# Optimization experiments

Measured on AMD Instinct MI355X. Metric: run time of the kernel, lower is better.

Reference implementation:

```python
import jax, jax.numpy as jnp
import numpy as np

B, N, D = 8, 2048, 1024


def setup_inputs() -> dict:
    key = jax.random.key(0)
    k1, k2, k3, k4 = jax.random.split(key, 4)
    x = jax.random.normal(k1, (B, N, D), dtype=jnp.float32)
    f = jax.random.normal(k2, (B, N, D), dtype=jnp.float32)
    # nn.Linear(D, 1, bias=False) weights, shape [1, D]
    lim = 1.0 / np.sqrt(D)
    wk = jax.random.uniform(k3, (1, D), dtype=jnp.float32, minval=-lim, maxval=lim)
    wq = jax.random.uniform(k4, (1, D), dtype=jnp.float32, minval=-lim, maxval=lim)
    return {"x": x, "f": f, "wk": wk, "wq": wq}


def reference(x, f, wk, wq):
    # scalar k/q projections: [B, N]
    k = jnp.einsum("bnd,d->bn", x, wk[0])
    q = jnp.einsum("bnd,d->bn", x, wq[0])
    scale = 1.0 / jnp.sqrt(jnp.float32(D))
    # rank-1 outer-product scores: e[b,i,j] = k[b,i]*q[b,j]/sqrt(D)
    e = k[:, :, None] * q[:, None, :] * scale  # [B, N, N]
    # keep upper triangle (incl. diag), then any exact zero -> -inf
    # (faithful to torch: e_post[e_post == 0] = -inf, which also hits
    #  naturally-zero upper-triangle entries)
    e_tri = jnp.triu(e)
    e_post = jnp.where(e_tri == 0, -jnp.inf, e_tri)
    a = jax.nn.softmax(e_post, axis=1)  # softmax over rows (dim=1)
    # f_out = a^T @ f
    f_out = jnp.einsum("bij,bid->bjd", a, f)
    return f_out
```

## Files before the change

### kernel.cpp

```cpp
#include <hip/hip_runtime.h>

#define B 8
#define N 2048
#define D 1024
#define SC 64
#define LC (N / SC)
#define M 6


__global__ __launch_bounds__(256) void k_pp(const float* __restrict__ x,
                                            const float* __restrict__ f,
                                            const float* __restrict__ wk,
                                            const float* __restrict__ wq,
                                            float* __restrict__ kq,
                                            float* __restrict__ part) {
    const int sc   = blockIdx.x & (SC - 1);
    const int b    = blockIdx.x >> 6;
    const int tid  = threadIdx.x;
    const int wave = tid >> 6;
    const int lane = tid & 63;

    __shared__ float sk[LC];

    {
        const float4* wk4 = (const float4*)wk;
        const float4* wq4 = (const float4*)wq;
        float4 kw[4], qw[4];
#pragma unroll
        for (int t = 0; t < 4; ++t) { kw[t] = wk4[t * 64 + lane]; qw[t] = wq4[t * 64 + lane]; }
#pragma unroll
        for (int r = 0; r < 8; ++r) {
            const int rl  = wave * 8 + r;
            const int row = b * N + sc * LC + rl;
            const float4* xr = (const float4*)(x + (size_t)row * D);
            float ak = 0.f, aq = 0.f;
#pragma unroll
            for (int t = 0; t < 4; ++t) {
                float4 xv = xr[t * 64 + lane];
                ak += xv.x * kw[t].x + xv.y * kw[t].y + xv.z * kw[t].z + xv.w * kw[t].w;
                aq += xv.x * qw[t].x + xv.y * qw[t].y + xv.z * qw[t].z + xv.w * qw[t].w;
            }
#pragma unroll
            for (int off = 32; off > 0; off >>= 1) {
                ak += __shfl_down(ak, off, 64);
                aq += __shfl_down(aq, off, 64);
            }
            if (lane == 0) {
                sk[rl] = ak;
                kq[row] = ak;
                kq[B * N + row] = aq;
            }
        }
    }
    __syncthreads();

    const float4* fb = (const float4*)(f + (size_t)(b * N + sc * LC) * D) + tid;
    float4 s[M];
#pragma unroll
    for (int m = 0; m < M; ++m) s[m] = make_float4(0.f, 0.f, 0.f, 0.f);
#pragma unroll 8
    for (int i = 0; i < LC; ++i) {
        float4 ff = fb[i * (D / 4)];
        float  kk = sk[i];
        float  w  = (kk != 0.0f) ? 1.0f : 0.0f;
        s[0].x += w * ff.x; s[0].y += w * ff.y; s[0].z += w * ff.z; s[0].w += w * ff.w;
        float kp = kk;
#pragma unroll
        for (int m = 1; m < M; ++m) {
            s[m].x += kp * ff.x; s[m].y += kp * ff.y;
            s[m].z += kp * ff.z; s[m].w += kp * ff.w;
            kp *= kk;
        }
    }
    float4* pb = (float4*)(part + (size_t)(b * SC + sc) * M * D) + tid;
#pragma unroll
    for (int m = 0; m < M; ++m) pb[m * (D / 4)] = s[m];
}

__global__ __launch_bounds__(256) void k_scan(float* __restrict__ part) {
    const int gid  = blockIdx.x * 256 + threadIdx.x;
    const int d    = gid & (D - 1);
    const int rest = gid >> 10;
    const int m    = rest % M;
    const int b    = rest / M;
    const size_t base = ((size_t)(b * SC) * M + m) * D + d;
    const size_t cs   = (size_t)M * D;
    float run = 0.f;
#pragma unroll 1
    for (int c0 = 0; c0 < SC; c0 += 8) {
        float buf[8];
#pragma unroll
        for (int j = 0; j < 8; ++j) buf[j] = part[base + (size_t)(c0 + j) * cs];
#pragma unroll
        for (int j = 0; j < 8; ++j) {
            float v = buf[j];
            part[base + (size_t)(c0 + j) * cs] = run;
            run += v;
        }
    }
}

__global__ __launch_bounds__(256) void k_out(const float* __restrict__ kq,
                                             const float* __restrict__ f,
                                             const float* __restrict__ part,
                                             float* __restrict__ out) {
    const int sc  = blockIdx.x & (SC - 1);
    const int b   = blockIdx.x >> 6;
    const int tid = threadIdx.x;

    __shared__ float sk[LC];
    __shared__ float sq[LC];
    __shared__ float sT[M];

    if (tid < 64) {
        float tm[M] = {0.f, 0.f, 0.f, 0.f, 0.f, 0.f};
        const float* kb = kq + b * N + tid * LC;
#pragma unroll
        for (int i = 0; i < LC; ++i) {
            float kk = kb[i];
            tm[0] += (kk != 0.0f) ? 1.0f : 0.0f;
            float kp = kk;
#pragma unroll
            for (int m = 1; m < M; ++m) { tm[m] += kp; kp *= kk; }
        }
#pragma unroll
        for (int m = 0; m < M; ++m) {
            float v = tm[m];
            const float orig = v;
#pragma unroll
            for (int off = 1; off < 64; off <<= 1) {
                float nv = __shfl_up(v, off, 64);
                if (tid >= off) v += nv;
            }
            if (tid == sc) sT[m] = v - orig;
        }
    } else if (tid < 64 + LC) {
        sk[tid - 64] = kq[b * N + sc * LC + (tid - 64)];
    } else if (tid >= 128 && tid < 128 + LC) {
        sq[tid - 128] = kq[B * N + b * N + sc * LC + (tid - 128)];
    }
    __syncthreads();

    float4 s[M];
    float  t[M];
    const float4* pb = (const float4*)(part + (size_t)(b * SC + sc) * M * D) + tid;
#pragma unroll
    for (int m = 0; m < M; ++m) s[m] = pb[m * (D / 4)];
#pragma unroll
    for (int m = 0; m < M; ++m) t[m] = sT[m];

    const float4* fb = (const float4*)(f + (size_t)(b * N + sc * LC) * D) + tid;
    float4*       ob = (float4*)(out + (size_t)(b * N + sc * LC) * D) + tid;

#pragma unroll 4
    for (int i = 0; i < LC; ++i) {
        float4 ff = fb[i * (D / 4)];
        float  kk = sk[i];
        float  qq = sq[i];
        float  w  = (kk != 0.0f) ? 1.0f : 0.0f;
        t[0] += w;
        s[0].x += w * ff.x; s[0].y += w * ff.y; s[0].z += w * ff.z; s[0].w += w * ff.w;
        float kp = kk;
#pragma unroll
        for (int m = 1; m < M; ++m) {
            t[m] += kp;
            s[m].x += kp * ff.x; s[m].y += kp * ff.y;
            s[m].z += kp * ff.z; s[m].w += kp * ff.w;
            kp *= kk;
        }
        const float cj = qq * 0.03125f;
        const float g2 = cj * 0.5f;
        const float g3 = cj * (1.0f / 3.0f);
        const float g4 = cj * 0.25f;
        const float g5 = cj * 0.2f;
        float Z = ((((t[5] * g5 + t[4]) * g4 + t[3]) * g3 + t[2]) * g2 + t[1]) * cj + t[0];
        float rz = __builtin_amdgcn_rcpf(Z);
        float4 o;
        o.x = (((((s[5].x * g5 + s[4].x) * g4 + s[3].x) * g3 + s[2].x) * g2 + s[1].x) * cj + s[0].x) * rz;
        o.y = (((((s[5].y * g5 + s[4].y) * g4 + s[3].y) * g3 + s[2].y) * g2 + s[1].y) * cj + s[0].y) * rz;
        o.z = (((((s[5].z * g5 + s[4].z) * g4 + s[3].z) * g3 + s[2].z) * g2 + s[1].z) * cj + s[0].z) * rz;
        o.w = (((((s[5].w * g5 + s[4].w) * g4 + s[3].w) * g3 + s[2].w) * g2 + s[1].w) * cj + s[0].w) * rz;
        ob[i * (D / 4)] = o;
    }
}

extern "C" void kernel_launch(void* const* d_in, const int* in_sizes, int n_in,
                              void* d_out, int out_size, void* d_ws, size_t ws_size,
                              hipStream_t stream) {
    (void)in_sizes; (void)n_in; (void)out_size; (void)ws_size;
    const float* x  = (const float*)d_in[0];
    const float* f  = (const float*)d_in[1];
    const float* wk = (const float*)d_in[2];
    const float* wq = (const float*)d_in[3];
    float* out = (float*)d_out;
    float* ws  = (float*)d_ws;

    float* kq   = ws;
    float* part = ws + 65536;

    hipLaunchKernelGGL(k_pp,   dim3(B * SC),           dim3(256), 0, stream, x, f, wk, wq, kq, part);
    hipLaunchKernelGGL(k_scan, dim3(B * M * D / 256),  dim3(256), 0, stream, part);
    hipLaunchKernelGGL(k_out,  dim3(B * SC),           dim3(256), 0, stream, kq, f, part, out);
}
```

Before: 196.8 us.

## Fuse prefix scan into output kernel and widen partial-sum kernel to 512 threads

Removes the separate scan kernel. The output kernel now sums all preceding chunk partials for its column, with the sequence regrouped into 16 larger row chunks and D split into 4 column quarters per block. The partial-sum kernel uses 512 threads with float2 accesses, so each block loads fewer rows of x per wave. This saves one launch and the read-modify-write pass over the partials. In exchange, later chunks read up to 60 partials redundantly, and the output kernel does scalar column accesses with longer serial row loops and fewer blocks.

Measured after the change: 239.5 us. +21.7%, slower.

```diff
diff --git a/kernel.cpp b/kernel.cpp
--- a/kernel.cpp
+++ b/kernel.cpp
@@ -5,15 +5,19 @@
 #define D 1024
 #define SC 64
 #define LC (N / SC)
+#define C2 16
+#define LR (N / C2)
+#define DQ 4
+#define COLS (D / DQ)
 #define M 6
 
 
-__global__ __launch_bounds__(256) void k_pp(const float* __restrict__ x,
-                                            const float* __restrict__ f,
-                                            const float* __restrict__ wk,
-                                            const float* __restrict__ wq,
-                                            float* __restrict__ kq,
-                                            float* __restrict__ part) {
+__global__ __launch_bounds__(512, 4) void k_pp(const float* __restrict__ x,
+                                               const float* __restrict__ f,
+                                               const float* __restrict__ wk,
+                                               const float* __restrict__ wq,
+                                               float* __restrict__ kq,
+                                               float* __restrict__ part) {
     const int sc   = blockIdx.x & (SC - 1);
     const int b    = blockIdx.x >> 6;
     const int tid  = threadIdx.x;
@@ -29,8 +33,8 @@
 #pragma unroll
         for (int t = 0; t < 4; ++t) { kw[t] = wk4[t * 64 + lane]; qw[t] = wq4[t * 64 + lane]; }
 #pragma unroll
-        for (int r = 0; r < 8; ++r) {
-            const int rl  = wave * 8 + r;
+        for (int r = 0; r < 4; ++r) {
+            const int rl  = wave * 4 + r;
             const int row = b * N + sc * LC + rl;
             const float4* xr = (const float4*)(x + (size_t)row * D);
             float ak = 0.f, aq = 0.f;
@@ -54,63 +58,44 @@
     }
     __syncthreads();
 
-    const float4* fb = (const float4*)(f + (size_t)(b * N + sc * LC) * D) + tid;
-    float4 s[M];
+    const float2* fb = (const float2*)(f + (size_t)(b * N + sc * LC) * D) + tid;
+    float2 s[M];
 #pragma unroll
-    for (int m = 0; m < M; ++m) s[m] = make_float4(0.f, 0.f, 0.f, 0.f);
+    for (int m = 0; m < M; ++m) s[m] = make_float2(0.f, 0.f);
 #pragma unroll 8
     for (int i = 0; i < LC; ++i) {
-        float4 ff = fb[i * (D / 4)];
+        float2 ff = fb[i * (D / 2)];
         float  kk = sk[i];
         float  w  = (kk != 0.0f) ? 1.0f : 0.0f;
-        s[0].x += w * ff.x; s[0].y += w * ff.y; s[0].z += w * ff.z; s[0].w += w * ff.w;
+        s[0].x += w * ff.x; s[0].y += w * ff.y;
         float kp = kk;
 #pragma unroll
         for (int m = 1; m < M; ++m) {
             s[m].x += kp * ff.x; s[m].y += kp * ff.y;
-            s[m].z += kp * ff.z; s[m].w += kp * ff.w;
             kp *= kk;
         }
     }
-    float4* pb = (float4*)(part + (size_t)(b * SC + sc) * M * D) + tid;
+    float2* pb = (float2*)(part + (size_t)(b * SC + sc) * M * D) + tid;
 #pragma unroll
-    for (int m = 0; m < M; ++m) pb[m * (D / 4)] = s[m];
+    for (int m = 0; m < M; ++m) pb[m * (D / 2)] = s[m];
 }
 
-__global__ __launch_bounds__(256) void k_scan(float* __restrict__ part) {
-    const int gid  = blockIdx.x * 256 + threadIdx.x;
-    const int d    = gid & (D - 1);
-    const int rest = gid >> 10;
-    const int m    = rest % M;
-    const int b    = rest / M;
-    const size_t base = ((size_t)(b * SC) * M + m) * D + d;
-    const size_t cs   = (size_t)M * D;
-    float run = 0.f;
-#pragma unroll 1
-    for (int c0 = 0; c0 < SC; c0 += 8) {
-        float buf[8];
-#pragma unroll
-        for (int j = 0; j < 8; ++j) buf[j] = part[base + (size_t)(c0 + j) * cs];
-#pragma unroll
-        for (int j = 0; j < 8; ++j) {
-            float v = buf[j];
-            part[base + (size_t)(c0 + j) * cs] = run;
-            run += v;
-        }
-    }
-}
-
-__global__ __launch_bounds__(256) void k_out(const float* __restrict__ kq,
-                                             const float* __restrict__ f,
-                                             const float* __restrict__ part,
-                                             float* __restrict__ out) {
-    const int sc  = blockIdx.x & (SC - 1);
+__global__ __launch_bounds__(256, 4) void k_so(const float* __restrict__ kq,
+                                               const float* __restrict__ f,
+                                               const float* __restrict__ part,
+                                               float* __restrict__ out) {
+    const int dq  = blockIdx.x & (DQ - 1);
+    const int c   = (blockIdx.x >> 2) & (C2 - 1);
     const int b   = blockIdx.x >> 6;
     const int tid = threadIdx.x;
+    const int col = dq * COLS + tid;
 
-    __shared__ float sk[LC];
-    __shared__ float sq[LC];
+    __shared__ float sk[LR];
+    __shared__ float sq[LR];
     __shared__ float sT[M];
+
+    if (tid < 128) sk[tid]       = kq[b * N + c * LR + tid];
+    else           sq[tid - 128] = kq[B * N + b * N + c * LR + (tid - 128)];
 
     if (tid < 64) {
         float tm[M] = {0.f, 0.f, 0.f, 0.f, 0.f, 0.f};
@@ -132,40 +117,41 @@
                 float nv = __shfl_up(v, off, 64);
                 if (tid >= off) v += nv;
             }
-            if (tid == sc) sT[m] = v - orig;
+            if (tid == 4 * c) sT[m] = v - orig;
         }
-    } else if (tid < 64 + LC) {
-        sk[tid - 64] = kq[b * N + sc * LC + (tid - 64)];
-    } else if (tid >= 128 && tid < 128 + LC) {
-        sq[tid - 128] = kq[B * N + b * N + sc * LC + (tid - 128)];
+    }
+
+    float run[M] = {0.f, 0.f, 0.f, 0.f, 0.f, 0.f};
+    {
+        const float* pbase = part + (size_t)(b * SC) * M * D + col;
+#pragma unroll 1
+        for (int p = 0; p < 4 * c; ++p) {
+            const float* rp = pbase + (size_t)p * (M * D);
+#pragma unroll
+            for (int m = 0; m < M; ++m) run[m] += rp[m * D];
+        }
     }
     __syncthreads();
 
-    float4 s[M];
-    float  t[M];
-    const float4* pb = (const float4*)(part + (size_t)(b * SC + sc) * M * D) + tid;
-#pragma unroll
-    for (int m = 0; m < M; ++m) s[m] = pb[m * (D / 4)];
+    float t[M];
 #pragma unroll
     for (int m = 0; m < M; ++m) t[m] = sT[m];
 
-    const float4* fb = (const float4*)(f + (size_t)(b * N + sc * LC) * D) + tid;
-    float4*       ob = (float4*)(out + (size_t)(b * N + sc * LC) * D) + tid;
-
+    const float* fb = f + (size_t)(b * N + c * LR) * D + col;
+    float*       ob = out + (size_t)(b * N + c * LR) * D + col;
 #pragma unroll 4
-    for (int i = 0; i < LC; ++i) {
-        float4 ff = fb[i * (D / 4)];
-        float  kk = sk[i];
-        float  qq = sq[i];
-        float  w  = (kk != 0.0f) ? 1.0f : 0.0f;
+    for (int i = 0; i < LR; ++i) {
+        float ff = fb[(size_t)i * D];
+        float kk = sk[i];
+        float qq = sq[i];
+        float w  = (kk != 0.0f) ? 1.0f : 0.0f;
         t[0] += w;
-        s[0].x += w * ff.x; s[0].y += w * ff.y; s[0].z += w * ff.z; s[0].w += w * ff.w;
+        run[0] += w * ff;
         float kp = kk;
 #pragma unroll
         for (int m = 1; m < M; ++m) {
             t[m] += kp;
-            s[m].x += kp * ff.x; s[m].y += kp * ff.y;
-            s[m].z += kp * ff.z; s[m].w += kp * ff.w;
+            run[m] += kp * ff;
             kp *= kk;
         }
         const float cj = qq * 0.03125f;
@@ -175,12 +161,8 @@
         const float g5 = cj * 0.2f;
         float Z = ((((t[5] * g5 + t[4]) * g4 + t[3]) * g3 + t[2]) * g2 + t[1]) * cj + t[0];
         float rz = __builtin_amdgcn_rcpf(Z);
-        float4 o;
-        o.x = (((((s[5].x * g5 + s[4].x) * g4 + s[3].x) * g3 + s[2].x) * g2 + s[1].x) * cj + s[0].x) * rz;
-        o.y = (((((s[5].y * g5 + s[4].y) * g4 + s[3].y) * g3 + s[2].y) * g2 + s[1].y) * cj + s[0].y) * rz;
-        o.z = (((((s[5].z * g5 + s[4].z) * g4 + s[3].z) * g3 + s[2].z) * g2 + s[1].z) * cj + s[0].z) * rz;
-        o.w = (((((s[5].w * g5 + s[4].w) * g4 + s[3].w) * g3 + s[2].w) * g2 + s[1].w) * cj + s[0].w) * rz;
-        ob[i * (D / 4)] = o;
+        ob[(size_t)i * D] =
+            (((((run[5] * g5 + run[4]) * g4 + run[3]) * g3 + run[2]) * g2 + run[1]) * cj + run[0]) * rz;
     }
 }
 
@@ -198,7 +180,6 @@
     float* kq   = ws;
     float* part = ws + 65536;
 
-    hipLaunchKernelGGL(k_pp,   dim3(B * SC),           dim3(256), 0, stream, x, f, wk, wq, kq, part);
-    hipLaunchKernelGGL(k_scan, dim3(B * M * D / 256),  dim3(256), 0, stream, part);
-    hipLaunchKernelGGL(k_out,  dim3(B * SC),           dim3(256), 0, stream, kq, f, part, out);
+    hipLaunchKernelGGL(k_pp, dim3(B * SC),       dim3(512), 0, stream, x, f, wk, wq, kq, part);
+    hipLaunchKernelGGL(k_so, dim3(B * C2 * DQ),  dim3(256), 0, stream, kq, f, part, out);
 }
```
